# Performance work log

Hardware: AMD Instinct MI355X
Metric: run time of the kernel (lower is better)

## Reference

```python
import jax, jax.numpy as jnp
import numpy as np

EMB = 1024
HEADS = 16
DEPTH = EMB // HEADS
B, S = 8, 1024


def setup_inputs() -> dict:
    key = jax.random.key(0)
    ks = jax.random.split(key, 12)
    sc = 0.02
    return {
        "q": jax.random.normal(ks[0], (B, S, EMB), jnp.float32),
        "k": jax.random.normal(ks[1], (B, S, EMB), jnp.float32),
        "v": jax.random.normal(ks[2], (B, S, EMB), jnp.float32),
        # per-head Dense weights stacked: [H, EMB, DEPTH], biases [H, DEPTH]
        "Wq": jax.random.normal(ks[3], (HEADS, EMB, DEPTH), jnp.float32) * sc,
        "bq": jnp.zeros((HEADS, DEPTH), jnp.float32),
        "Wk": jax.random.normal(ks[4], (HEADS, EMB, DEPTH), jnp.float32) * sc,
        "bk": jnp.zeros((HEADS, DEPTH), jnp.float32),
        "Wv": jax.random.normal(ks[5], (HEADS, EMB, DEPTH), jnp.float32) * sc,
        "bv": jnp.zeros((HEADS, DEPTH), jnp.float32),
        # output Dense: [EMB, EMB], bias [EMB]
        "Wo": jax.random.normal(ks[6], (EMB, EMB), jnp.float32) * sc,
        "bo": jnp.zeros((EMB,), jnp.float32),
    }


def reference(q, k, v, Wq, bq, Wk, bk, Wv, bv, Wo, bo):
    # Per-head Dense projections, batched over heads via einsum.
    # qh: [B, H, S, DEPTH]
    qh = jnp.einsum("bsd,hde->bhse", q, Wq) + bq[None, :, None, :]
    kh = jnp.einsum("bsd,hde->bhse", k, Wk) + bk[None, :, None, :]
    vh = jnp.einsum("bsd,hde->bhse", v, Wv) + bv[None, :, None, :]
    # Scaled dot-product attention per head: logits [B, H, Sq, Sk]
    scale = 1.0 / jnp.sqrt(jnp.asarray(DEPTH, jnp.float32))
    logits = jnp.einsum("bhqe,bhke->bhqk", qh, kh) * scale
    attn = jax.nn.softmax(logits, axis=-1)
    ctx = jnp.einsum("bhqk,bhke->bhqe", attn, vh)  # [B, H, S, DEPTH]
    # concat heads along last axis (head order preserved)
    ctx = jnp.transpose(ctx, (0, 2, 1, 3)).reshape(B, S, EMB)
    return ctx @ Wo + bo
```

## Files before the change

kernel.cpp:

```cpp
#include <hip/hip_runtime.h>
#include <hip/hip_bf16.h>
#include <stdint.h>

typedef __bf16 bf16;
typedef __attribute__((ext_vector_type(8))) __bf16 bf16x8;
typedef __attribute__((ext_vector_type(4))) __bf16 bf16x4;
typedef __attribute__((ext_vector_type(4))) float f32x4;

#define GLD(g, l) __builtin_amdgcn_global_load_lds( \
    (const __attribute__((address_space(1))) void*)(g), \
    (__attribute__((address_space(3))) void*)(l), 16, 0, 0)

__device__ __forceinline__ f32x4 mfma16(bf16x8 a, bf16x8 b, f32x4 c) {
  return __builtin_amdgcn_mfma_f32_16x16x32_bf16(a, b, c, 0, 0, 0);
}
__device__ __forceinline__ float fexp2(float x) {
  return __builtin_amdgcn_exp2f(x);
}

__global__ void wtrans3(const float* __restrict__ Wq, const float* __restrict__ Wk,
                        const float* __restrict__ Wv, bf16* __restrict__ WT)
{
  __shared__ bf16 t[32][33];
  const int w = blockIdx.z;
  const float* W = (w == 0) ? Wq : (w == 1) ? Wk : Wv;
  const int h = blockIdx.x >> 1;
  const int c0 = (blockIdx.x & 1) * 32;
  const int r0 = blockIdx.y * 32;
  const float* s = W + (size_t)h * 65536;
  bf16* d = WT + (size_t)w * (1 << 20) + (size_t)h * 65536;
  const int tx = threadIdx.x, ty = threadIdx.y;
#pragma unroll
  for (int i = 0; i < 32; i += 8)
    t[ty + i][tx] = (bf16)s[(r0 + ty + i) * 64 + c0 + tx];
  __syncthreads();
#pragma unroll
  for (int i = 0; i < 32; i += 8)
    d[(c0 + ty + i) * 1024 + r0 + tx] = t[tx][ty + i];
}

__global__ void wtransO(const float* __restrict__ src, bf16* __restrict__ dst)
{
  __shared__ bf16 t[32][33];
  const int c0 = blockIdx.x * 32, r0 = blockIdx.y * 32;
  const int tx = threadIdx.x, ty = threadIdx.y;
#pragma unroll
  for (int i = 0; i < 32; i += 8)
    t[ty + i][tx] = (bf16)src[(r0 + ty + i) * 1024 + c0 + tx];
  __syncthreads();
#pragma unroll
  for (int i = 0; i < 32; i += 8)
    dst[(c0 + ty + i) * 1024 + r0 + tx] = t[tx][ty + i];
}

__global__ __launch_bounds__(256) void cast2(const float* __restrict__ q,
                                             const float* __restrict__ k,
                                             bf16* __restrict__ qc,
                                             bf16* __restrict__ kc)
{
  const float* s = blockIdx.y ? k : q;
  bf16* d = blockIdx.y ? kc : qc;
  const size_t i = ((size_t)blockIdx.x * 256 + threadIdx.x) * 8;
  float4 a = *(const float4*)(s + i);
  float4 b = *(const float4*)(s + i + 4);
  bf16x8 p;
  p[0] = (bf16)a.x; p[1] = (bf16)a.y; p[2] = (bf16)a.z; p[3] = (bf16)a.w;
  p[4] = (bf16)b.x; p[5] = (bf16)b.y; p[6] = (bf16)b.z; p[7] = (bf16)b.w;
  *(bf16x8*)(d + i) = p;
}

__global__ __launch_bounds__(256) void proj_qkv(
    const bf16* __restrict__ qc, const bf16* __restrict__ kc,
    const float* __restrict__ v, const bf16* __restrict__ WT,
    const float* __restrict__ bq, const float* __restrict__ bk,
    const float* __restrict__ bv, bf16* __restrict__ qh,
    bf16* __restrict__ kh, bf16* __restrict__ vt, float cscale)
{
  __shared__ bf16 S[16384];
  const int tid = threadIdx.x;
  const int wave = tid >> 6, lane = tid & 63;
  const int lr = lane & 15, quad = lane >> 4, kq = quad * 8;
  const int n0 = blockIdx.y * 128;
  const int mseg = blockIdx.x * 128;
  const int seg = mseg >> 13;
  const int m0 = mseg & 8191;
  const int wr = (wave >> 1) * 64, wc = (wave & 1) * 64;

  const float* bias = (seg == 0) ? bq : (seg == 1) ? bk : bv;
  const bf16* Bt = WT + (size_t)seg * (1 << 20);

  f32x4 acc[4][4];
#pragma unroll
  for (int i = 0; i < 4; i++)
#pragma unroll
    for (int j = 0; j < 4; j++)
#pragma unroll
      for (int e = 0; e < 4; e++) acc[i][j][e] = 0.f;

  const int srow = tid >> 2;
  const int sko = (tid & 3) * 8;
  const bf16* bPtr = Bt + (size_t)(n0 + srow) * 1024 + sko;

  if (seg < 2) {
    const bf16* Ab = (seg == 1) ? kc : qc;
    const bf16* aPtr = Ab + (size_t)(m0 + srow) * 1024 + sko;
    GLD(aPtr,             S + tid * 8);
    GLD(aPtr + 64 * 1024, S + 2048 + tid * 8);
    GLD(bPtr,             S + 4096 + tid * 8);
    GLD(bPtr + 64 * 1024, S + 6144 + tid * 8);
    for (int it = 0; it < 32; ++it) {
      const int p = it & 1;
      bf16* buf = S + p * 8192;
      bf16* nbuf = S + (p ^ 1) * 8192;
      __syncthreads();
      if (it + 1 < 32) {
        const int k0 = (it + 1) * 32;
        GLD(aPtr + k0,             nbuf + tid * 8);
        GLD(aPtr + 64 * 1024 + k0, nbuf + 2048 + tid * 8);
        GLD(bPtr + k0,             nbuf + 4096 + tid * 8);
        GLD(bPtr + 64 * 1024 + k0, nbuf + 6144 + tid * 8);
      }
      bf16x8 af[4], bfr[4];
#pragma unroll
      for (int i = 0; i < 4; i++) {
        af[i]  = *(const bf16x8*)(buf + (wr + i * 16 + lr) * 32 + kq);
        bfr[i] = *(const bf16x8*)(buf + 4096 + (wc + i * 16 + lr) * 32 + kq);
      }
#pragma unroll
      for (int im = 0; im < 4; im++)
#pragma unroll
        for (int in = 0; in < 4; in++)
          acc[im][in] = mfma16(af[im], bfr[in], acc[im][in]);
    }
  } else {
    const int ar = tid >> 1, ac2 = (tid & 1) * 16;
    const float* vPtr = v + (size_t)(m0 + ar) * 1024 + ac2;
    float4 f[4];
#pragma unroll
    for (int j = 0; j < 4; j++) f[j] = *(const float4*)(vPtr + j * 4);
    {
      bf16x8 p0, p1;
      p0[0]=(bf16)f[0].x; p0[1]=(bf16)f[0].y; p0[2]=(bf16)f[0].z; p0[3]=(bf16)f[0].w;
      p0[4]=(bf16)f[1].x; p0[5]=(bf16)f[1].y; p0[6]=(bf16)f[1].z; p0[7]=(bf16)f[1].w;
      p1[0]=(bf16)f[2].x; p1[1]=(bf16)f[2].y; p1[2]=(bf16)f[2].z; p1[3]=(bf16)f[2].w;
      p1[4]=(bf16)f[3].x; p1[5]=(bf16)f[3].y; p1[6]=(bf16)f[3].z; p1[7]=(bf16)f[3].w;
      *(bf16x8*)(S + ar * 32 + ac2)     = p0;
      *(bf16x8*)(S + ar * 32 + ac2 + 8) = p1;
    }
    GLD(bPtr,             S + 4096 + tid * 8);
    GLD(bPtr + 64 * 1024, S + 6144 + tid * 8);
    for (int it = 0; it < 32; ++it) {
      const int p = it & 1;
      bf16* buf = S + p * 8192;
      bf16* nbuf = S + (p ^ 1) * 8192;
      __syncthreads();
      const bool more = (it + 1 < 32);
      if (more) {
        const int k0 = (it + 1) * 32;
        GLD(bPtr + k0,             nbuf + 4096 + tid * 8);
        GLD(bPtr + 64 * 1024 + k0, nbuf + 6144 + tid * 8);
#pragma unroll
        for (int j = 0; j < 4; j++) f[j] = *(const float4*)(vPtr + k0 + j * 4);
      }
      bf16x8 af[4], bfr[4];
#pragma unroll
      for (int i = 0; i < 4; i++) {
        af[i]  = *(const bf16x8*)(buf + (wr + i * 16 + lr) * 32 + kq);
        bfr[i] = *(const bf16x8*)(buf + 4096 + (wc + i * 16 + lr) * 32 + kq);
      }
#pragma unroll
      for (int im = 0; im < 4; im++)
#pragma unroll
        for (int in = 0; in < 4; in++)
          acc[im][in] = mfma16(af[im], bfr[in], acc[im][in]);
      if (more) {
        bf16x8 p0, p1;
        p0[0]=(bf16)f[0].x; p0[1]=(bf16)f[0].y; p0[2]=(bf16)f[0].z; p0[3]=(bf16)f[0].w;
        p0[4]=(bf16)f[1].x; p0[5]=(bf16)f[1].y; p0[6]=(bf16)f[1].z; p0[7]=(bf16)f[1].w;
        p1[0]=(bf16)f[2].x; p1[1]=(bf16)f[2].y; p1[2]=(bf16)f[2].z; p1[3]=(bf16)f[2].w;
        p1[4]=(bf16)f[3].x; p1[5]=(bf16)f[3].y; p1[6]=(bf16)f[3].z; p1[7]=(bf16)f[3].w;
        *(bf16x8*)(nbuf + ar * 32 + ac2)     = p0;
        *(bf16x8*)(nbuf + ar * 32 + ac2 + 8) = p1;
      }
    }
  }

  const int qd = quad * 4;
  float bv4[4];
#pragma unroll
  for (int in = 0; in < 4; in++) bv4[in] = bias[n0 + wc + in * 16 + lr];

  if (seg < 2) {
    bf16* C = (seg == 0) ? qh : kh;
    const float cmul = (seg == 0) ? cscale : 1.0f;
#pragma unroll
    for (int im = 0; im < 4; im++) {
      const int row = m0 + wr + im * 16 + qd;
#pragma unroll
      for (int in = 0; in < 4; in++) {
        const int col = n0 + wc + in * 16 + lr;
#pragma unroll
        for (int i = 0; i < 4; i++)
          C[(size_t)(row + i) * 1024 + col] = (bf16)((acc[im][in][i] + bv4[in]) * cmul);
      }
    }
  } else {
#pragma unroll
    for (int im = 0; im < 4; im++) {
      const int row = m0 + wr + im * 16 + qd;
      const int b = row >> 10, sin = row & 1023;
#pragma unroll
      for (int in = 0; in < 4; in++) {
        const int col = n0 + wc + in * 16 + lr;
        const int h = col >> 6, e = col & 63;
        bf16x4 pk;
#pragma unroll
        for (int i = 0; i < 4; i++) pk[i] = (bf16)(acc[im][in][i] + bv4[in]);
        *(bf16x4*)(vt + (size_t)(b * 16 + h) * 65536 + e * 1024 + sin) = pk;
      }
    }
  }
}

__global__ __launch_bounds__(256) void gemm_a16_c32(
    const bf16* __restrict__ A, const bf16* __restrict__ Bt,
    const float* __restrict__ bias, float* __restrict__ C)
{
  __shared__ bf16 S[16384];
  const int tid = threadIdx.x;
  const int wave = tid >> 6, lane = tid & 63;
  const int lr = lane & 15, kq = ((lane >> 4)) * 8;
  const int m0 = blockIdx.x * 128, n0 = blockIdx.y * 128;
  const int wr = (wave >> 1) * 64, wc = (wave & 1) * 64;

  f32x4 acc[4][4];
#pragma unroll
  for (int i = 0; i < 4; i++)
#pragma unroll
    for (int j = 0; j < 4; j++)
#pragma unroll
      for (int e = 0; e < 4; e++) acc[i][j][e] = 0.f;

  const int srow = tid >> 2;
  const int sko = (tid & 3) * 8;
  const bf16* aPtr = A + (size_t)(m0 + srow) * 1024 + sko;
  const bf16* bPtr = Bt + (size_t)(n0 + srow) * 1024 + sko;

  GLD(aPtr,             S + tid * 8);
  GLD(aPtr + 64 * 1024, S + 2048 + tid * 8);
  GLD(bPtr,             S + 4096 + tid * 8);
  GLD(bPtr + 64 * 1024, S + 6144 + tid * 8);
  for (int it = 0; it < 32; ++it) {
    const int p = it & 1;
    bf16* buf = S + p * 8192;
    bf16* nbuf = S + (p ^ 1) * 8192;
    __syncthreads();
    if (it + 1 < 32) {
      const int k0 = (it + 1) * 32;
      GLD(aPtr + k0,             nbuf + tid * 8);
      GLD(aPtr + 64 * 1024 + k0, nbuf + 2048 + tid * 8);
      GLD(bPtr + k0,             nbuf + 4096 + tid * 8);
      GLD(bPtr + 64 * 1024 + k0, nbuf + 6144 + tid * 8);
    }
    bf16x8 af[4], bfr[4];
#pragma unroll
    for (int i = 0; i < 4; i++) {
      af[i]  = *(const bf16x8*)(buf + (wr + i * 16 + lr) * 32 + kq);
      bfr[i] = *(const bf16x8*)(buf + 4096 + (wc + i * 16 + lr) * 32 + kq);
    }
#pragma unroll
    for (int im = 0; im < 4; im++)
#pragma unroll
      for (int in = 0; in < 4; in++)
        acc[im][in] = mfma16(af[im], bfr[in], acc[im][in]);
  }

  const int qd = ((tid & 63) >> 4) * 4;
  float bv4[4];
#pragma unroll
  for (int in = 0; in < 4; in++) bv4[in] = bias[n0 + wc + in * 16 + lr];
#pragma unroll
  for (int im = 0; im < 4; im++) {
    const int row = m0 + wr + im * 16 + qd;
#pragma unroll
    for (int in = 0; in < 4; in++) {
      const int col = n0 + wc + in * 16 + lr;
#pragma unroll
      for (int i = 0; i < 4; i++)
        C[(size_t)(row + i) * 1024 + col] = acc[im][in][i] + bv4[in];
    }
  }
}

__global__ __launch_bounds__(256) void attn_k(
    const bf16* Q, const bf16* __restrict__ Kh,
    const bf16* __restrict__ Vt, bf16* O)
{
  __shared__ bf16 sK[64 * 72];
  __shared__ bf16 sV[64 * 72];
  __shared__ bf16 sP[128 * 72];
  const int h = blockIdx.x, b = blockIdx.y, q0 = blockIdx.z * 128;
  const int tid = threadIdx.x, wave = tid >> 6, lane = tid & 63;
  const int lr = lane & 15, quad = lane >> 4, kq = quad * 8;
  const int wq = wave * 32;

  const bf16* Qb = Q + (size_t)(b * 1024 + q0) * 1024 + h * 64;
  const bf16* Kb = Kh + (size_t)(b * 1024) * 1024 + h * 64;
  const bf16* Vb = Vt + (size_t)(b * 16 + h) * 65536;

  bf16x8 qf[2][2];
#pragma unroll
  for (int rg = 0; rg < 2; rg++)
#pragma unroll
    for (int ks = 0; ks < 2; ks++)
      qf[rg][ks] = *(const bf16x8*)(Qb + (wq + rg * 16 + lr) * 1024 + ks * 32 + kq);

  f32x4 o[2][4];
  float rsum[2][4];
#pragma unroll
  for (int rg = 0; rg < 2; rg++) {
#pragma unroll
    for (int et = 0; et < 4; et++)
#pragma unroll
      for (int e = 0; e < 4; e++) o[rg][et][e] = 0.f;
#pragma unroll
    for (int i = 0; i < 4; i++) rsum[rg][i] = 0.f;
  }

  const int r = tid >> 3;
  const int c = (tid & 7) * 8;

  bf16x8 k1 = *(const bf16x8*)(Kb + (size_t)r * 1024 + c);
  bf16x8 k2 = *(const bf16x8*)(Kb + (size_t)(32 + r) * 1024 + c);
  bf16x8 v1 = *(const bf16x8*)(Vb + (size_t)r * 1024 + c);
  bf16x8 v2 = *(const bf16x8*)(Vb + (size_t)(32 + r) * 1024 + c);

  for (int kv0 = 0; kv0 < 1024; kv0 += 64) {
    __syncthreads();
    *(bf16x8*)(sK + r * 72 + c) = k1;
    *(bf16x8*)(sK + (32 + r) * 72 + c) = k2;
    *(bf16x8*)(sV + r * 72 + c) = v1;
    *(bf16x8*)(sV + (32 + r) * 72 + c) = v2;
    __syncthreads();
    if (kv0 + 64 < 1024) {
      k1 = *(const bf16x8*)(Kb + (size_t)(kv0 + 64 + r) * 1024 + c);
      k2 = *(const bf16x8*)(Kb + (size_t)(kv0 + 96 + r) * 1024 + c);
      v1 = *(const bf16x8*)(Vb + (size_t)r * 1024 + kv0 + 64 + c);
      v2 = *(const bf16x8*)(Vb + (size_t)(32 + r) * 1024 + kv0 + 64 + c);
    }

    f32x4 sc[2][4];
#pragma unroll
    for (int nt = 0; nt < 4; nt++) {
      bf16x8 kf0 = *(const bf16x8*)(sK + (nt * 16 + lr) * 72 + kq);
      bf16x8 kf1 = *(const bf16x8*)(sK + (nt * 16 + lr) * 72 + 32 + kq);
#pragma unroll
      for (int rg = 0; rg < 2; rg++) {
        f32x4 z;
#pragma unroll
        for (int e = 0; e < 4; e++) z[e] = 0.f;
        z = mfma16(qf[rg][0], kf0, z);
        z = mfma16(qf[rg][1], kf1, z);
        sc[rg][nt] = z;
      }
    }

#pragma unroll
    for (int rg = 0; rg < 2; rg++)
#pragma unroll
      for (int i = 0; i < 4; i++) {
        float p0 = fexp2(sc[rg][0][i]);
        float p1 = fexp2(sc[rg][1][i]);
        float p2 = fexp2(sc[rg][2][i]);
        float p3 = fexp2(sc[rg][3][i]);
        rsum[rg][i] += (p0 + p1) + (p2 + p3);
        const int prow = (wq + rg * 16 + quad * 4 + i) * 72;
        sP[prow + 0 * 16 + lr] = (bf16)p0;
        sP[prow + 1 * 16 + lr] = (bf16)p1;
        sP[prow + 2 * 16 + lr] = (bf16)p2;
        sP[prow + 3 * 16 + lr] = (bf16)p3;
      }
    __syncthreads();

#pragma unroll
    for (int et = 0; et < 4; et++) {
      bf16x8 vf0 = *(const bf16x8*)(sV + (et * 16 + lr) * 72 + kq);
      bf16x8 vf1 = *(const bf16x8*)(sV + (et * 16 + lr) * 72 + 32 + kq);
#pragma unroll
      for (int rg = 0; rg < 2; rg++) {
        bf16x8 pa = *(const bf16x8*)(sP + (wq + rg * 16 + lr) * 72 + kq);
        bf16x8 pb = *(const bf16x8*)(sP + (wq + rg * 16 + lr) * 72 + 32 + kq);
        o[rg][et] = mfma16(pa, vf0, o[rg][et]);
        o[rg][et] = mfma16(pb, vf1, o[rg][et]);
      }
    }
  }

#pragma unroll
  for (int rg = 0; rg < 2; rg++)
#pragma unroll
    for (int i = 0; i < 4; i++) {
      float rs = rsum[rg][i];
#pragma unroll
      for (int off = 1; off < 16; off <<= 1)
        rs += __shfl_xor(rs, off, 64);
      rsum[rg][i] = 1.f / rs;
    }

  bf16* Ob = O + (size_t)(b * 1024 + q0) * 1024 + h * 64;
#pragma unroll
  for (int rg = 0; rg < 2; rg++)
#pragma unroll
    for (int i = 0; i < 4; i++) {
      const int row = wq + rg * 16 + quad * 4 + i;
#pragma unroll
      for (int et = 0; et < 4; et++)
        Ob[row * 1024 + et * 16 + lr] = (bf16)(o[rg][et][i] * rsum[rg][i]);
    }
}

extern "C" void kernel_launch(void* const* d_in, const int* in_sizes, int n_in,
                              void* d_out, int out_size, void* d_ws, size_t ws_size,
                              hipStream_t stream)
{
  const float* q  = (const float*)d_in[0];
  const float* k  = (const float*)d_in[1];
  const float* v  = (const float*)d_in[2];
  const float* Wq = (const float*)d_in[3];
  const float* bq = (const float*)d_in[4];
  const float* Wk = (const float*)d_in[5];
  const float* bk = (const float*)d_in[6];
  const float* Wv = (const float*)d_in[7];
  const float* bv = (const float*)d_in[8];
  const float* Wo = (const float*)d_in[9];
  const float* bo = (const float*)d_in[10];
  float* out = (float*)d_out;
  bf16* ws = (bf16*)d_ws;

  const int MB = 1 << 20;
  bf16* WT  = ws;
  bf16* qh  = ws + 3 * MB;
  bf16* kh  = ws + 11 * MB;
  bf16* vt  = ws + 19 * MB;
  bf16* WoT = ws + 27 * MB;
  bf16* qc  = (bf16*)d_out;
  bf16* kc  = (bf16*)d_out + 8 * MB;

  const float cscale = 0.1803368801111601f;

  dim3 tb(32, 8);
  wtrans3<<<dim3(32, 32, 3), tb, 0, stream>>>(Wq, Wk, Wv, WT);
  wtransO<<<dim3(32, 32), tb, 0, stream>>>(Wo, WoT);
  cast2<<<dim3(4096, 2), 256, 0, stream>>>(q, k, qc, kc);

  proj_qkv<<<dim3(192, 8), 256, 0, stream>>>(qc, kc, v, WT, bq, bk, bv,
                                             qh, kh, vt, cscale);

  attn_k<<<dim3(16, 8, 8), 256, 0, stream>>>(qh, kh, vt, qh);

  gemm_a16_c32<<<dim3(64, 8), 256, 0, stream>>>(qh, WoT, bo, out);
}
```

Before: 337.1 us.

## Deepen GEMM pipelines to four LDS stages with swizzled layout and raised MFMA priority

The projection and output GEMMs move from double-buffered LDS to a four-slot ring with three tiles in flight. Each iteration waits with an explicit vmcnt plus a raw barrier instead of __syncthreads. Shared-memory tiles get an XOR swizzle on the 8-element column chunks to cut bank conflicts on the fragment reads. MFMA blocks run at raised wave priority. LDS use doubles to 64KB per block, which may lower occupancy, and the hand-written waitcnt counts must match the in-flight loads exactly.

Result: no change. 332.3 us (-1.4%).

```diff
diff --git a/kernel.cpp b/kernel.cpp
--- a/kernel.cpp
+++ b/kernel.cpp
@@ -17,6 +17,38 @@
 __device__ __forceinline__ float fexp2(float x) {
   return __builtin_amdgcn_exp2f(x);
 }
+__device__ __forceinline__ bf16x8 cvt8(const float4& a, const float4& b) {
+  bf16x8 p;
+  p[0] = (bf16)a.x; p[1] = (bf16)a.y; p[2] = (bf16)a.z; p[3] = (bf16)a.w;
+  p[4] = (bf16)b.x; p[5] = (bf16)b.y; p[6] = (bf16)b.z; p[7] = (bf16)b.w;
+  return p;
+}
+
+__device__ __forceinline__ void compute128(const bf16* buf, int wr, int wc,
+                                           int lr, int quad,
+                                           f32x4 (&acc)[4][4]) {
+  bf16x8 af[4], bfr[4];
+#pragma unroll
+  for (int i = 0; i < 4; i++) {
+    const int ra = wr + i * 16 + lr;
+    const int rb = wc + i * 16 + lr;
+    af[i]  = *(const bf16x8*)(buf + ra * 32 + ((quad ^ ((ra >> 1) & 3)) * 8));
+    bfr[i] = *(const bf16x8*)(buf + 4096 + rb * 32 +
+                              ((quad ^ ((rb >> 1) & 3)) * 8));
+  }
+  __builtin_amdgcn_s_setprio(1);
+#pragma unroll
+  for (int im = 0; im < 4; im++)
+#pragma unroll
+    for (int in = 0; in < 4; in++)
+      acc[im][in] = mfma16(af[im], bfr[in], acc[im][in]);
+  __builtin_amdgcn_s_setprio(0);
+}
+
+#define WAIT_BAR(cnt)                                            \
+  asm volatile("s_waitcnt vmcnt(" #cnt ")" ::: "memory");        \
+  __builtin_amdgcn_s_barrier();                                  \
+  asm volatile("" ::: "memory")
 
 __global__ void wtrans3(const float* __restrict__ Wq, const float* __restrict__ Wk,
                         const float* __restrict__ Wv, bf16* __restrict__ WT)
@@ -63,10 +95,7 @@
   const size_t i = ((size_t)blockIdx.x * 256 + threadIdx.x) * 8;
   float4 a = *(const float4*)(s + i);
   float4 b = *(const float4*)(s + i + 4);
-  bf16x8 p;
-  p[0] = (bf16)a.x; p[1] = (bf16)a.y; p[2] = (bf16)a.z; p[3] = (bf16)a.w;
-  p[4] = (bf16)b.x; p[5] = (bf16)b.y; p[6] = (bf16)b.z; p[7] = (bf16)b.w;
-  *(bf16x8*)(d + i) = p;
+  *(bf16x8*)(d + i) = cvt8(a, b);
 }
 
 __global__ __launch_bounds__(256) void proj_qkv(
@@ -76,10 +105,10 @@
     const float* __restrict__ bv, bf16* __restrict__ qh,
     bf16* __restrict__ kh, bf16* __restrict__ vt, float cscale)
 {
-  __shared__ bf16 S[16384];
+  __shared__ bf16 S[32768];
   const int tid = threadIdx.x;
   const int wave = tid >> 6, lane = tid & 63;
-  const int lr = lane & 15, quad = lane >> 4, kq = quad * 8;
+  const int lr = lane & 15, quad = lane >> 4;
   const int n0 = blockIdx.y * 128;
   const int mseg = blockIdx.x * 128;
   const int seg = mseg >> 13;
@@ -98,89 +127,76 @@
       for (int e = 0; e < 4; e++) acc[i][j][e] = 0.f;
 
   const int srow = tid >> 2;
-  const int sko = (tid & 3) * 8;
+  const int sko = ((tid & 3) ^ ((srow >> 1) & 3)) * 8;
   const bf16* bPtr = Bt + (size_t)(n0 + srow) * 1024 + sko;
 
   if (seg < 2) {
     const bf16* Ab = (seg == 1) ? kc : qc;
     const bf16* aPtr = Ab + (size_t)(m0 + srow) * 1024 + sko;
-    GLD(aPtr,             S + tid * 8);
-    GLD(aPtr + 64 * 1024, S + 2048 + tid * 8);
-    GLD(bPtr,             S + 4096 + tid * 8);
-    GLD(bPtr + 64 * 1024, S + 6144 + tid * 8);
-    for (int it = 0; it < 32; ++it) {
-      const int p = it & 1;
-      bf16* buf = S + p * 8192;
-      bf16* nbuf = S + (p ^ 1) * 8192;
-      __syncthreads();
-      if (it + 1 < 32) {
-        const int k0 = (it + 1) * 32;
-        GLD(aPtr + k0,             nbuf + tid * 8);
-        GLD(aPtr + 64 * 1024 + k0, nbuf + 2048 + tid * 8);
-        GLD(bPtr + k0,             nbuf + 4096 + tid * 8);
-        GLD(bPtr + 64 * 1024 + k0, nbuf + 6144 + tid * 8);
-      }
-      bf16x8 af[4], bfr[4];
-#pragma unroll
-      for (int i = 0; i < 4; i++) {
-        af[i]  = *(const bf16x8*)(buf + (wr + i * 16 + lr) * 32 + kq);
-        bfr[i] = *(const bf16x8*)(buf + 4096 + (wc + i * 16 + lr) * 32 + kq);
-      }
-#pragma unroll
-      for (int im = 0; im < 4; im++)
-#pragma unroll
-        for (int in = 0; in < 4; in++)
-          acc[im][in] = mfma16(af[im], bfr[in], acc[im][in]);
-    }
+#pragma unroll
+    for (int t = 0; t < 3; ++t) {
+      bf16* nb = S + t * 8192;
+      GLD(aPtr + t * 32,             nb + tid * 8);
+      GLD(aPtr + 64 * 1024 + t * 32, nb + 2048 + tid * 8);
+      GLD(bPtr + t * 32,             nb + 4096 + tid * 8);
+      GLD(bPtr + 64 * 1024 + t * 32, nb + 6144 + tid * 8);
+    }
+    for (int it = 0; it < 29; ++it) {
+      WAIT_BAR(8);
+      const int k0 = (it + 3) * 32;
+      bf16* nb = S + ((it + 3) & 3) * 8192;
+      GLD(aPtr + k0,             nb + tid * 8);
+      GLD(aPtr + 64 * 1024 + k0, nb + 2048 + tid * 8);
+      GLD(bPtr + k0,             nb + 4096 + tid * 8);
+      GLD(bPtr + 64 * 1024 + k0, nb + 6144 + tid * 8);
+      compute128(S + (it & 3) * 8192, wr, wc, lr, quad, acc);
+    }
+    WAIT_BAR(8);
+    compute128(S + ((29) & 3) * 8192, wr, wc, lr, quad, acc);
+    WAIT_BAR(4);
+    compute128(S + ((30) & 3) * 8192, wr, wc, lr, quad, acc);
+    WAIT_BAR(0);
+    compute128(S + ((31) & 3) * 8192, wr, wc, lr, quad, acc);
   } else {
-    const int ar = tid >> 1, ac2 = (tid & 1) * 16;
-    const float* vPtr = v + (size_t)(m0 + ar) * 1024 + ac2;
+    const int ar = tid >> 1, acb = (tid & 1) * 2;
+    const int asw = (ar >> 1) & 3;
+    const float* vPtr = v + (size_t)(m0 + ar) * 1024 + acb * 8;
     float4 f[4];
 #pragma unroll
     for (int j = 0; j < 4; j++) f[j] = *(const float4*)(vPtr + j * 4);
     {
-      bf16x8 p0, p1;
-      p0[0]=(bf16)f[0].x; p0[1]=(bf16)f[0].y; p0[2]=(bf16)f[0].z; p0[3]=(bf16)f[0].w;
-      p0[4]=(bf16)f[1].x; p0[5]=(bf16)f[1].y; p0[6]=(bf16)f[1].z; p0[7]=(bf16)f[1].w;
-      p1[0]=(bf16)f[2].x; p1[1]=(bf16)f[2].y; p1[2]=(bf16)f[2].z; p1[3]=(bf16)f[2].w;
-      p1[4]=(bf16)f[3].x; p1[5]=(bf16)f[3].y; p1[6]=(bf16)f[3].z; p1[7]=(bf16)f[3].w;
-      *(bf16x8*)(S + ar * 32 + ac2)     = p0;
-      *(bf16x8*)(S + ar * 32 + ac2 + 8) = p1;
-    }
-    GLD(bPtr,             S + 4096 + tid * 8);
-    GLD(bPtr + 64 * 1024, S + 6144 + tid * 8);
+      *(bf16x8*)(S + ar * 32 + ((acb ^ asw) * 8))       = cvt8(f[0], f[1]);
+      *(bf16x8*)(S + ar * 32 + (((acb + 1) ^ asw) * 8)) = cvt8(f[2], f[3]);
+    }
+    GLD(bPtr,                  S + 4096 + tid * 8);
+    GLD(bPtr + 64 * 1024,      S + 6144 + tid * 8);
+    GLD(bPtr + 32,             S + 8192 + 4096 + tid * 8);
+    GLD(bPtr + 64 * 1024 + 32, S + 8192 + 6144 + tid * 8);
+    GLD(bPtr + 64,             S + 16384 + 4096 + tid * 8);
+    GLD(bPtr + 64 * 1024 + 64, S + 16384 + 6144 + tid * 8);
+    asm volatile("s_waitcnt vmcnt(4)" ::: "memory");
     for (int it = 0; it < 32; ++it) {
-      const int p = it & 1;
-      bf16* buf = S + p * 8192;
-      bf16* nbuf = S + (p ^ 1) * 8192;
-      __syncthreads();
-      const bool more = (it + 1 < 32);
-      if (more) {
+      asm volatile("s_waitcnt lgkmcnt(0)" ::: "memory");
+      __builtin_amdgcn_sched_barrier(0);
+      __builtin_amdgcn_s_barrier();
+      asm volatile("" ::: "memory");
+      const bool moreA = (it + 1 < 32);
+      if (moreA) {
         const int k0 = (it + 1) * 32;
-        GLD(bPtr + k0,             nbuf + 4096 + tid * 8);
-        GLD(bPtr + 64 * 1024 + k0, nbuf + 6144 + tid * 8);
 #pragma unroll
         for (int j = 0; j < 4; j++) f[j] = *(const float4*)(vPtr + k0 + j * 4);
       }
-      bf16x8 af[4], bfr[4];
-#pragma unroll
-      for (int i = 0; i < 4; i++) {
-        af[i]  = *(const bf16x8*)(buf + (wr + i * 16 + lr) * 32 + kq);
-        bfr[i] = *(const bf16x8*)(buf + 4096 + (wc + i * 16 + lr) * 32 + kq);
-      }
-#pragma unroll
-      for (int im = 0; im < 4; im++)
-#pragma unroll
-        for (int in = 0; in < 4; in++)
-          acc[im][in] = mfma16(af[im], bfr[in], acc[im][in]);
-      if (more) {
-        bf16x8 p0, p1;
-        p0[0]=(bf16)f[0].x; p0[1]=(bf16)f[0].y; p0[2]=(bf16)f[0].z; p0[3]=(bf16)f[0].w;
-        p0[4]=(bf16)f[1].x; p0[5]=(bf16)f[1].y; p0[6]=(bf16)f[1].z; p0[7]=(bf16)f[1].w;
-        p1[0]=(bf16)f[2].x; p1[1]=(bf16)f[2].y; p1[2]=(bf16)f[2].z; p1[3]=(bf16)f[2].w;
-        p1[4]=(bf16)f[3].x; p1[5]=(bf16)f[3].y; p1[6]=(bf16)f[3].z; p1[7]=(bf16)f[3].w;
-        *(bf16x8*)(nbuf + ar * 32 + ac2)     = p0;
-        *(bf16x8*)(nbuf + ar * 32 + ac2 + 8) = p1;
+      if (it + 3 < 32) {
+        const int k0 = (it + 3) * 32;
+        bf16* nb = S + ((it + 3) & 3) * 8192;
+        GLD(bPtr + k0,             nb + 4096 + tid * 8);
+        GLD(bPtr + 64 * 1024 + k0, nb + 6144 + tid * 8);
+      }
+      compute128(S + (it & 3) * 8192, wr, wc, lr, quad, acc);
+      if (moreA) {
+        bf16* nb = S + ((it + 1) & 3) * 8192;
+        *(bf16x8*)(nb + ar * 32 + ((acb ^ asw) * 8))       = cvt8(f[0], f[1]);
+        *(bf16x8*)(nb + ar * 32 + (((acb + 1) ^ asw) * 8)) = cvt8(f[2], f[3]);
       }
     }
   }
@@ -226,10 +242,10 @@
     const bf16* __restrict__ A, const bf16* __restrict__ Bt,
     const float* __restrict__ bias, float* __restrict__ C)
 {
-  __shared__ bf16 S[16384];
+  __shared__ bf16 S[32768];
   const int tid = threadIdx.x;
   const int wave = tid >> 6, lane = tid & 63;
-  const int lr = lane & 15, kq = ((lane >> 4)) * 8;
+  const int lr = lane & 15, quad = lane >> 4;
   const int m0 = blockIdx.x * 128, n0 = blockIdx.y * 128;
   const int wr = (wave >> 1) * 64, wc = (wave & 1) * 64;
 
@@ -242,40 +258,36 @@
       for (int e = 0; e < 4; e++) acc[i][j][e] = 0.f;
 
   const int srow = tid >> 2;
-  const int sko = (tid & 3) * 8;
+  const int sko = ((tid & 3) ^ ((srow >> 1) & 3)) * 8;
   const bf16* aPtr = A + (size_t)(m0 + srow) * 1024 + sko;
   const bf16* bPtr = Bt + (size_t)(n0 + srow) * 1024 + sko;
 
-  GLD(aPtr,             S + tid * 8);
-  GLD(aPtr + 64 * 1024, S + 2048 + tid * 8);
-  GLD(bPtr,             S + 4096 + tid * 8);
-  GLD(bPtr + 64 * 1024, S + 6144 + tid * 8);
-  for (int it = 0; it < 32; ++it) {
-    const int p = it & 1;
-    bf16* buf = S + p * 8192;
-    bf16* nbuf = S + (p ^ 1) * 8192;
-    __syncthreads();
-    if (it + 1 < 32) {
-      const int k0 = (it + 1) * 32;
-      GLD(aPtr + k0,             nbuf + tid * 8);
-      GLD(aPtr + 64 * 1024 + k0, nbuf + 2048 + tid * 8);
-      GLD(bPtr + k0,             nbuf + 4096 + tid * 8);
-      GLD(bPtr + 64 * 1024 + k0, nbuf + 6144 + tid * 8);
-    }
-    bf16x8 af[4], bfr[4];
-#pragma unroll
-    for (int i = 0; i < 4; i++) {
-      af[i]  = *(const bf16x8*)(buf + (wr + i * 16 + lr) * 32 + kq);
-      bfr[i] = *(const bf16x8*)(buf + 4096 + (wc + i * 16 + lr) * 32 + kq);
-    }
-#pragma unroll
-    for (int im = 0; im < 4; im++)
-#pragma unroll
-      for (int in = 0; in < 4; in++)
-        acc[im][in] = mfma16(af[im], bfr[in], acc[im][in]);
-  }
-
-  const int qd = ((tid & 63) >> 4) * 4;
+#pragma unroll
+  for (int t = 0; t < 3; ++t) {
+    bf16* nb = S + t * 8192;
+    GLD(aPtr + t * 32,             nb + tid * 8);
+    GLD(aPtr + 64 * 1024 + t * 32, nb + 2048 + tid * 8);
+    GLD(bPtr + t * 32,             nb + 4096 + tid * 8);
+    GLD(bPtr + 64 * 1024 + t * 32, nb + 6144 + tid * 8);
+  }
+  for (int it = 0; it < 29; ++it) {
+    WAIT_BAR(8);
+    const int k0 = (it + 3) * 32;
+    bf16* nb = S + ((it + 3) & 3) * 8192;
+    GLD(aPtr + k0,             nb + tid * 8);
+    GLD(aPtr + 64 * 1024 + k0, nb + 2048 + tid * 8);
+    GLD(bPtr + k0,             nb + 4096 + tid * 8);
+    GLD(bPtr + 64 * 1024 + k0, nb + 6144 + tid * 8);
+    compute128(S + (it & 3) * 8192, wr, wc, lr, quad, acc);
+  }
+  WAIT_BAR(8);
+  compute128(S + ((29) & 3) * 8192, wr, wc, lr, quad, acc);
+  WAIT_BAR(4);
+  compute128(S + ((30) & 3) * 8192, wr, wc, lr, quad, acc);
+  WAIT_BAR(0);
+  compute128(S + ((31) & 3) * 8192, wr, wc, lr, quad, acc);
+
+  const int qd = quad * 4;
   float bv4[4];
 #pragma unroll
   for (int in = 0; in < 4; in++) bv4[in] = bias[n0 + wc + in * 16 + lr];
```
